# Kernel tuning notes

Measured on AMD Instinct MI355X. Metric: run time of the kernel, lower is better.

The kernel has to match this reference:

```python
import jax, jax.numpy as jnp
import numpy as np


def setup_inputs() -> dict:
    key = jax.random.key(0)
    ks = jax.random.split(key, 6)
    B, S, D_IN, D_OUT, E, R = 4, 2048, 4096, 4096, 8, 16
    x = jax.random.normal(ks[0], (B, S, D_IN), dtype=jnp.float32)
    probs = jax.random.uniform(ks[1], (B, E), dtype=jnp.float32)
    router_probs = probs / jnp.sum(probs, axis=-1, keepdims=True)
    weight = jax.random.normal(ks[2], (D_OUT, D_IN), dtype=jnp.float32) * 0.02
    bias = jax.random.normal(ks[3], (D_OUT,), dtype=jnp.float32) * 0.02
    lora_A = jax.random.normal(ks[4], (E, R, D_IN), dtype=jnp.float32) * 0.02
    lora_B = jax.random.normal(ks[5], (E, D_OUT, R), dtype=jnp.float32) * 0.02
    return {"x": x, "router_probs": router_probs, "weight": weight,
            "bias": bias, "lora_A": lora_A, "lora_B": lora_B}


def reference(x, router_probs, weight, bias, lora_A, lora_B):
    scaling = 2.0
    # base linear: [b,s,i] @ [o,i]^T + bias
    base_out = jnp.einsum('bsi,oi->bso', x, weight) + bias
    # low-rank per-expert projection: [b,s,e,r] (small: r=16)
    mid = jnp.einsum('bsi,eri->bser', x, lora_A)
    # weight by router probs (per batch, per expert) before up-projection
    mid_w = mid * router_probs[:, None, :, None]
    # sum over experts fused into the up-projection contraction
    delta = jnp.einsum('bser,eor->bso', mid_w, lora_B) * scaling
    return base_out + delta
```

## Files before the change

kernel.cpp:

```cpp
#include <hip/hip_runtime.h>


typedef _Float16 half8 __attribute__((ext_vector_type(8)));
typedef _Float16 half4 __attribute__((ext_vector_type(4)));
typedef float    f32x4 __attribute__((ext_vector_type(4)));

#define M_TOT 8192
#define N_TOT 4096
#define K_IN  4096
#define KA    4224
#define NT    132

__device__ __forceinline__ void cvt_store4(_Float16* p, float4 f) {
  half4 h;
  h[0] = (_Float16)f.x; h[1] = (_Float16)f.y;
  h[2] = (_Float16)f.z; h[3] = (_Float16)f.w;
  *(half4*)p = h;
}

template <int LOG2C, int DCOLS>
__global__ __launch_bounds__(256) void convert_f32_f16_t(
    const float* __restrict__ src, _Float16* __restrict__ dst, int total8) {
  for (int i = blockIdx.x * 256 + threadIdx.x; i < total8;
       i += gridDim.x * 256) {
    int base = i << 3;
    int r = base >> LOG2C;
    int c = base & ((1 << LOG2C) - 1);
    const float4* s = (const float4*)(src + (size_t)base);
    float4 f0 = s[0], f1 = s[1];
    half8 h;
    h[0]=(_Float16)f0.x; h[1]=(_Float16)f0.y; h[2]=(_Float16)f0.z; h[3]=(_Float16)f0.w;
    h[4]=(_Float16)f1.x; h[5]=(_Float16)f1.y; h[6]=(_Float16)f1.z; h[7]=(_Float16)f1.w;
    *(half8*)(dst + (size_t)r * DCOLS + c) = h;
  }
}

__global__ __launch_bounds__(256) void wtail_gather_f16(
    const float* __restrict__ loraB, _Float16* __restrict__ Wa) {
  int idx = blockIdx.x * 256 + threadIdx.x;
  int n = idx >> 7, j = idx & 127;
  int e = j >> 4, r = j & 15;
  Wa[(size_t)n * KA + K_IN + j] =
      (_Float16)loraB[((size_t)e * N_TOT + n) * 16 + r];
}

__global__ __launch_bounds__(256) void lorabf_gather_f32(
    const float* __restrict__ loraB, float* __restrict__ lorabf) {
  int idx = blockIdx.x * 256 + threadIdx.x;
  int n = idx >> 7, j = idx & 127;
  int e = j >> 4, r = j & 15;
  lorabf[(size_t)n * 128 + j] = loraB[((size_t)e * N_TOT + n) * 16 + r];
}

__global__ __launch_bounds__(256) void mid2_kernel(
    _Float16* __restrict__ Xa, const _Float16* __restrict__ lAh,
    const float* __restrict__ router) {
  __shared__ _Float16 As[32 * 64];
  __shared__ _Float16 Bs[128 * 64];
  int tid = threadIdx.x, lane = tid & 63, w = tid >> 6;
  int m0 = blockIdx.x * 32;
  int b = m0 >> 11;
  f32x4 acc[2][2] = {};

  for (int ks = 0; ks < 64; ++ks) {
    int kb = ks * 128;
    {
      const char* s = (const char*)Xa +
          (size_t)(m0 + w * 8 + (lane >> 3)) * (KA * 2) + kb + (lane & 7) * 16;
      __builtin_amdgcn_global_load_lds(
          (const __attribute__((address_space(1))) void*)s,
          (__attribute__((address_space(3))) void*)((char*)As + w * 1024), 16, 0, 0);
    }
#pragma unroll
    for (int i = 0; i < 4; ++i) {
      const char* s = (const char*)lAh +
          (size_t)((w * 4 + i) * 8 + (lane >> 3)) * (4096 * 2) + kb + (lane & 7) * 16;
      __builtin_amdgcn_global_load_lds(
          (const __attribute__((address_space(1))) void*)s,
          (__attribute__((address_space(3))) void*)((char*)Bs + (w * 4 + i) * 1024), 16, 0, 0);
    }
    __syncthreads();
#pragma unroll
    for (int kk = 0; kk < 2; ++kk) {
      half8 a[2], bf[2];
#pragma unroll
      for (int mi = 0; mi < 2; ++mi)
        a[mi] = *(const half8*)(As + (mi * 16 + (lane & 15)) * 64 + kk * 32 + (lane >> 4) * 8);
#pragma unroll
      for (int ni = 0; ni < 2; ++ni)
        bf[ni] = *(const half8*)(Bs + (w * 32 + ni * 16 + (lane & 15)) * 64 + kk * 32 + (lane >> 4) * 8);
#pragma unroll
      for (int mi = 0; mi < 2; ++mi)
#pragma unroll
        for (int ni = 0; ni < 2; ++ni)
          acc[mi][ni] = __builtin_amdgcn_mfma_f32_16x16x32_f16(a[mi], bf[ni], acc[mi][ni], 0, 0, 0);
    }
    __syncthreads();
  }

#pragma unroll
  for (int ni = 0; ni < 2; ++ni) {
    int j = w * 32 + ni * 16 + (lane & 15);
    int e = j >> 4;
    float sc = 2.0f * router[b * 8 + e];
#pragma unroll
    for (int mi = 0; mi < 2; ++mi) {
      f32x4 v = acc[mi][ni];
#pragma unroll
      for (int jj = 0; jj < 4; ++jj) {
        int m = m0 + mi * 16 + (lane >> 4) * 4 + jj;
        Xa[(size_t)m * KA + K_IN + j] = (_Float16)(v[jj] * sc);
      }
    }
  }
}

__global__ __launch_bounds__(256) void mid_kernel(
    const float* __restrict__ x, const float* __restrict__ loraA,
    const float* __restrict__ router, float* __restrict__ midw) {
  __shared__ _Float16 As[32 * 64];
  __shared__ _Float16 Bs[128 * 64];
  int tid = threadIdx.x, lane = tid & 63, w = tid >> 6;
  int m0 = blockIdx.x * 32;
  int b = m0 >> 11;
  f32x4 acc[2][2] = {};
  for (int ks = 0; ks < 64; ++ks) {
    int k0 = ks * 64;
#pragma unroll
    for (int it = 0; it < 2; ++it) {
      int idx = tid + it * 256;
      int r = idx >> 4, c4 = idx & 15;
      float4 f = *(const float4*)(x + (size_t)(m0 + r) * K_IN + k0 + c4 * 4);
      cvt_store4(As + r * 64 + c4 * 4, f);
    }
#pragma unroll
    for (int it = 0; it < 8; ++it) {
      int idx = tid + it * 256;
      int r = idx >> 4, c4 = idx & 15;
      float4 f = *(const float4*)(loraA + (size_t)r * K_IN + k0 + c4 * 4);
      cvt_store4(Bs + r * 64 + c4 * 4, f);
    }
    __syncthreads();
#pragma unroll
    for (int kk = 0; kk < 2; ++kk) {
      half8 a[2], bf[2];
#pragma unroll
      for (int mi = 0; mi < 2; ++mi)
        a[mi] = *(const half8*)(As + (mi * 16 + (lane & 15)) * 64 + kk * 32 + (lane >> 4) * 8);
#pragma unroll
      for (int ni = 0; ni < 2; ++ni)
        bf[ni] = *(const half8*)(Bs + (w * 32 + ni * 16 + (lane & 15)) * 64 + kk * 32 + (lane >> 4) * 8);
#pragma unroll
      for (int mi = 0; mi < 2; ++mi)
#pragma unroll
        for (int ni = 0; ni < 2; ++ni)
          acc[mi][ni] = __builtin_amdgcn_mfma_f32_16x16x32_f16(a[mi], bf[ni], acc[mi][ni], 0, 0, 0);
    }
    __syncthreads();
  }
#pragma unroll
  for (int ni = 0; ni < 2; ++ni) {
    int j = w * 32 + ni * 16 + (lane & 15);
    int e = j >> 4;
    float sc = 2.0f * router[b * 8 + e];
#pragma unroll
    for (int mi = 0; mi < 2; ++mi) {
      f32x4 v = acc[mi][ni];
#pragma unroll
      for (int jj = 0; jj < 4; ++jj) {
        int m = m0 + mi * 16 + (lane >> 4) * 4 + jj;
        midw[(size_t)m * 128 + j] = v[jj] * sc;
      }
    }
  }
}

#define BAR    __builtin_amdgcn_s_barrier()
#define SCHED0 __builtin_amdgcn_sched_barrier(0)
#define PRIO1  __builtin_amdgcn_s_setprio(1)
#define PRIO0  __builtin_amdgcn_s_setprio(0)
#define VMW0   asm volatile("s_waitcnt vmcnt(0)" ::: "memory")
#define GLOAD(src, dst) __builtin_amdgcn_global_load_lds( \
    (const __attribute__((address_space(1))) void*)(src), \
    (__attribute__((address_space(3))) void*)(dst), 16, 0, 0)

#define READS(AF, BF, SL) do { \
  _Pragma("unroll") for (int ni = 0; ni < 4; ++ni) \
    BF[ni] = *(const half8*)(LDS + 65536 + (SL) * 16384 + \
                             (wn + ni * 16 + ln15) * 64 + rslot); \
  _Pragma("unroll") for (int mi = 0; mi < 8; ++mi) \
    AF[mi] = *(const half8*)(LDS + (SL) * 16384 + \
                             (wm + mi * 16 + ln15) * 64 + rslot); \
  } while (0)

#define STAGE4(TT, SL) do { \
  const char* sA_ = XpC + (size_t)(TT) * 64; \
  const char* sB_ = WpC + (size_t)(TT) * 64; \
  GLOAD(sA_ + goff0, LDS + (SL) * 16384 + l0); \
  GLOAD(sA_ + goff1, LDS + (SL) * 16384 + l1); \
  GLOAD(sB_ + goff0, LDS + 65536 + (SL) * 16384 + l0); \
  GLOAD(sB_ + goff1, LDS + 65536 + (SL) * 16384 + l1); \
  } while (0)

#define MFMA32(AF, BF) do { \
  PRIO1; \
  _Pragma("unroll") for (int mi = 0; mi < 8; ++mi) \
    _Pragma("unroll") for (int ni = 0; ni < 4; ++ni) \
      acc[mi][ni] = __builtin_amdgcn_mfma_f32_16x16x32_f16( \
          AF[mi], BF[ni], acc[mi][ni], 0, 0, 0); \
  PRIO0; \
  } while (0)

#define TILE_NB(AF, BF, SL) do { READS(AF, BF, SL); MFMA32(AF, BF); } while (0)

__global__ __launch_bounds__(512, 2) void gemm256(
    const _Float16* __restrict__ Xa, const _Float16* __restrict__ Wa,
    const float* __restrict__ bias, float* __restrict__ out) {
  __shared__ __align__(16) char LDS[131072];

  int tid = threadIdx.x, lane = tid & 63, w = tid >> 6;
  int ln15 = lane & 15, ln4 = lane >> 4;
  int wm = (w >> 2) * 128, wn = (w & 3) * 64;

  int bid = blockIdx.x;
  int xcd = bid & 7, idx = bid >> 3;
  int mt = (xcd & 3) * 8 + (idx & 7);
  int nt = (xcd >> 2) * 8 + (idx >> 3);
  int m0 = mt << 8, n0 = nt << 8;

  const char* XpC = (const char*)Xa + (size_t)m0 * (KA * 2);
  const char* WpC = (const char*)Wa + (size_t)n0 * (KA * 2);

  int i0 = tid, i1 = tid + 512;
  int goff0 = (i0 >> 2) * (KA * 2) + (((i0 & 3) ^ ((i0 >> 3) & 3)) * 16);
  int goff1 = (i1 >> 2) * (KA * 2) + (((i1 & 3) ^ ((i1 >> 3) & 3)) * 16);
  int l0 = i0 * 16, l1 = i1 * 16;

  int rslot = ((ln4 ^ ((lane >> 1) & 3)) * 16);

  f32x4 acc[8][4] = {};
  half8 aE[8], bE[4], aO[8], bO[4];

  STAGE4(0, 0); STAGE4(1, 1);

#pragma unroll 1
  for (int t4 = 0; t4 < NT; t4 += 4) {
    VMW0; BAR; SCHED0;
    STAGE4(t4 + 2, 2); STAGE4(t4 + 3, 3);
    TILE_NB(aE, bE, 0);
    TILE_NB(aO, bO, 1);
    VMW0; BAR; SCHED0;
    if (t4 + 4 < NT) { STAGE4(t4 + 4, 0); STAGE4(t4 + 5, 1); }
    TILE_NB(aE, bE, 2);
    TILE_NB(aO, bO, 3);
  }

#pragma unroll
  for (int ni = 0; ni < 4; ++ni) {
    int n = n0 + wn + ni * 16 + ln15;
    float bz = bias[n];
#pragma unroll
    for (int mi = 0; mi < 8; ++mi) {
      f32x4 v = acc[mi][ni];
      int mb = m0 + wm + mi * 16 + ln4 * 4;
#pragma unroll
      for (int jj = 0; jj < 4; ++jj)
        out[(size_t)(mb + jj) * N_TOT + n] = v[jj] + bz;
    }
  }
}

__global__ __launch_bounds__(256) void gemm_fallback(
    const float* __restrict__ x, const float* __restrict__ wgt,
    const float* __restrict__ midw, const float* __restrict__ lorabf,
    const float* __restrict__ bias, float* __restrict__ out) {
  __shared__ _Float16 As[128 * 64];
  __shared__ _Float16 Bs[128 * 64];
  int tid = threadIdx.x, lane = tid & 63, w = tid >> 6;
  int mt = blockIdx.x & 63, nt = blockIdx.x >> 6;
  int m0 = mt << 7, n0 = nt << 7;
  int wm = (w >> 1) * 64, wn = (w & 1) * 64;
  f32x4 acc[4][4] = {};
  for (int ks = 0; ks < 66; ++ks) {
    int k0 = ks * 64;
    const float *asrc, *bsrc; size_t astr, bstr; int ac, bc;
    if (ks < 64) { asrc = x;    astr = K_IN; ac = k0;        bsrc = wgt;    bstr = K_IN; bc = k0; }
    else         { asrc = midw; astr = 128;  ac = k0 - K_IN; bsrc = lorabf; bstr = 128;  bc = k0 - K_IN; }
#pragma unroll
    for (int it = 0; it < 8; ++it) {
      int idx = tid + it * 256;
      int r = idx >> 4, c4 = idx & 15;
      float4 fa = *(const float4*)(asrc + (size_t)(m0 + r) * astr + ac + c4 * 4);
      cvt_store4(As + r * 64 + c4 * 4, fa);
      float4 fb = *(const float4*)(bsrc + (size_t)(n0 + r) * bstr + bc + c4 * 4);
      cvt_store4(Bs + r * 64 + c4 * 4, fb);
    }
    __syncthreads();
#pragma unroll
    for (int kk = 0; kk < 2; ++kk) {
      half8 a[4], bf[4];
#pragma unroll
      for (int mi = 0; mi < 4; ++mi)
        a[mi] = *(const half8*)(As + (wm + mi * 16 + (lane & 15)) * 64 + kk * 32 + (lane >> 4) * 8);
#pragma unroll
      for (int ni = 0; ni < 4; ++ni)
        bf[ni] = *(const half8*)(Bs + (wn + ni * 16 + (lane & 15)) * 64 + kk * 32 + (lane >> 4) * 8);
#pragma unroll
      for (int mi = 0; mi < 4; ++mi)
#pragma unroll
        for (int ni = 0; ni < 4; ++ni)
          acc[mi][ni] = __builtin_amdgcn_mfma_f32_16x16x32_f16(a[mi], bf[ni], acc[mi][ni], 0, 0, 0);
    }
    __syncthreads();
  }
#pragma unroll
  for (int ni = 0; ni < 4; ++ni) {
    int n = n0 + wn + ni * 16 + (lane & 15);
    float bz = bias[n];
#pragma unroll
    for (int mi = 0; mi < 4; ++mi) {
      f32x4 v = acc[mi][ni];
      int mbase = m0 + wm + mi * 16 + (lane >> 4) * 4;
#pragma unroll
      for (int jj = 0; jj < 4; ++jj)
        out[(size_t)(mbase + jj) * N_TOT + n] = v[jj] + bz;
    }
  }
}

extern "C" void kernel_launch(void* const* d_in, const int* in_sizes, int n_in,
                              void* d_out, int out_size, void* d_ws, size_t ws_size,
                              hipStream_t stream) {
  const float* x      = (const float*)d_in[0];
  const float* router = (const float*)d_in[1];
  const float* wgt    = (const float*)d_in[2];
  const float* bias   = (const float*)d_in[3];
  const float* loraA  = (const float*)d_in[4];
  const float* loraB  = (const float*)d_in[5];
  float* out = (float*)d_out;
  char* ws = (char*)d_ws;

  const size_t XAUG_B = (size_t)M_TOT * KA * 2;
  const size_t WAUG_B = (size_t)N_TOT * KA * 2;
  const size_t LAH_B  = (size_t)128 * K_IN * 2;
  const size_t MIDW_B = (size_t)M_TOT * 128 * 4;
  bool fast = ws_size >= XAUG_B + WAUG_B + LAH_B;

  if (fast) {
    _Float16* Xa  = (_Float16*)ws;
    _Float16* Wa  = (_Float16*)(ws + XAUG_B);
    _Float16* lAh = (_Float16*)(ws + XAUG_B + WAUG_B);
    convert_f32_f16_t<12, KA><<<2048, 256, 0, stream>>>(x,   Xa, M_TOT * K_IN / 8);
    convert_f32_f16_t<12, KA><<<2048, 256, 0, stream>>>(wgt, Wa, N_TOT * K_IN / 8);
    convert_f32_f16_t<12, 4096><<<256, 256, 0, stream>>>(loraA, lAh, 128 * K_IN / 8);
    wtail_gather_f16<<<2048, 256, 0, stream>>>(loraB, Wa);
    mid2_kernel<<<256, 256, 0, stream>>>(Xa, lAh, router);
    gemm256<<<512, 512, 0, stream>>>(Xa, Wa, bias, out);
  } else {
    float* midw   = (float*)ws;
    float* lorabf = (float*)(ws + MIDW_B);
    lorabf_gather_f32<<<2048, 256, 0, stream>>>(loraB, lorabf);
    mid_kernel<<<256, 256, 0, stream>>>(x, loraA, router, midw);
    gemm_fallback<<<2048, 256, 0, stream>>>(x, wgt, midw, lorabf, bias, out);
  }
}
```

Measured before the change: 379.2 us.

## Stream GEMM B operand from global to registers and deepen A LDS pipeline

In the main GEMM kernel, the weight (B) tiles now load straight from global memory into registers one tile ahead. Only the activation (A) tiles are staged through LDS, in a four-slot ring with one barrier per k-tile, and LDS shrinks to 64KB. A fragments are read in two halves to save registers. Separately, the mid2 kernel gets an XOR-swizzled LDS layout to cut bank conflicts on its fragment reads. The trade-off is that waves sharing a column block now fetch B redundantly from cache. The loop also relies on implicit compiler waitcnts, not explicit vmcnt waits, to order the LDS-bound loads.

After: 486.8 us. 28.4% more time.

```diff
diff --git a/kernel.cpp b/kernel.cpp
--- a/kernel.cpp
+++ b/kernel.cpp
@@ -62,33 +62,37 @@
   int b = m0 >> 11;
   f32x4 acc[2][2] = {};
 
+  int scol = ((lane & 7) ^ (lane >> 3)) * 16;
+  int ln15 = lane & 15, ln4 = lane >> 4;
+
   for (int ks = 0; ks < 64; ++ks) {
     int kb = ks * 128;
     {
       const char* s = (const char*)Xa +
-          (size_t)(m0 + w * 8 + (lane >> 3)) * (KA * 2) + kb + (lane & 7) * 16;
+          (size_t)(m0 + w * 8 + (lane >> 3)) * (KA * 2) + kb + scol;
       __builtin_amdgcn_global_load_lds(
           (const __attribute__((address_space(1))) void*)s,
-          (__attribute__((address_space(3))) void*)((char*)As + w * 1024), 16, 0, 0);
+          (__attribute__((address_space(3))) void*)((char*)As + w * 1024 + lane * 16), 16, 0, 0);
     }
 #pragma unroll
     for (int i = 0; i < 4; ++i) {
       const char* s = (const char*)lAh +
-          (size_t)((w * 4 + i) * 8 + (lane >> 3)) * (4096 * 2) + kb + (lane & 7) * 16;
+          (size_t)((w * 4 + i) * 8 + (lane >> 3)) * (4096 * 2) + kb + scol;
       __builtin_amdgcn_global_load_lds(
           (const __attribute__((address_space(1))) void*)s,
-          (__attribute__((address_space(3))) void*)((char*)Bs + (w * 4 + i) * 1024), 16, 0, 0);
+          (__attribute__((address_space(3))) void*)((char*)Bs + (w * 4 + i) * 1024 + lane * 16), 16, 0, 0);
     }
     __syncthreads();
 #pragma unroll
     for (int kk = 0; kk < 2; ++kk) {
+      int rs = (((kk * 4 + ln4) ^ (ln15 & 7)) << 4);
       half8 a[2], bf[2];
 #pragma unroll
       for (int mi = 0; mi < 2; ++mi)
-        a[mi] = *(const half8*)(As + (mi * 16 + (lane & 15)) * 64 + kk * 32 + (lane >> 4) * 8);
+        a[mi] = *(const half8*)((const char*)As + (mi * 16 + ln15) * 128 + rs);
 #pragma unroll
       for (int ni = 0; ni < 2; ++ni)
-        bf[ni] = *(const half8*)(Bs + (w * 32 + ni * 16 + (lane & 15)) * 64 + kk * 32 + (lane >> 4) * 8);
+        bf[ni] = *(const half8*)((const char*)Bs + (w * 32 + ni * 16 + ln15) * 128 + rs);
 #pragma unroll
       for (int mi = 0; mi < 2; ++mi)
 #pragma unroll
@@ -100,7 +104,7 @@
 
 #pragma unroll
   for (int ni = 0; ni < 2; ++ni) {
-    int j = w * 32 + ni * 16 + (lane & 15);
+    int j = w * 32 + ni * 16 + ln15;
     int e = j >> 4;
     float sc = 2.0f * router[b * 8 + e];
 #pragma unroll
@@ -108,7 +112,7 @@
       f32x4 v = acc[mi][ni];
 #pragma unroll
       for (int jj = 0; jj < 4; ++jj) {
-        int m = m0 + mi * 16 + (lane >> 4) * 4 + jj;
+        int m = m0 + mi * 16 + ln4 * 4 + jj;
         Xa[(size_t)m * KA + K_IN + j] = (_Float16)(v[jj] * sc);
       }
     }
@@ -179,44 +183,52 @@
 #define SCHED0 __builtin_amdgcn_sched_barrier(0)
 #define PRIO1  __builtin_amdgcn_s_setprio(1)
 #define PRIO0  __builtin_amdgcn_s_setprio(0)
-#define VMW0   asm volatile("s_waitcnt vmcnt(0)" ::: "memory")
+#define VMW4   asm volatile("s_waitcnt vmcnt(4)" ::: "memory")
 #define GLOAD(src, dst) __builtin_amdgcn_global_load_lds( \
     (const __attribute__((address_space(1))) void*)(src), \
     (__attribute__((address_space(3))) void*)(dst), 16, 0, 0)
 
-#define READS(AF, BF, SL) do { \
+#define READ_A4(mb, SL) do { \
+  _Pragma("unroll") for (int i = 0; i < 4; ++i) \
+    aF[i] = *(const half8*)(LDS + (SL) * 16384 + \
+                            (wm + ((mb) + i) * 16 + ln15) * 64 + rslot); \
+  } while (0)
+
+#define LOADB(BF, TT) do { \
+  const char* sB_ = WpC + (size_t)(TT) * 64; \
   _Pragma("unroll") for (int ni = 0; ni < 4; ++ni) \
-    BF[ni] = *(const half8*)(LDS + 65536 + (SL) * 16384 + \
-                             (wn + ni * 16 + ln15) * 64 + rslot); \
-  _Pragma("unroll") for (int mi = 0; mi < 8; ++mi) \
-    AF[mi] = *(const half8*)(LDS + (SL) * 16384 + \
-                             (wm + mi * 16 + ln15) * 64 + rslot); \
-  } while (0)
-
-#define STAGE4(TT, SL) do { \
+    BF[ni] = *(const half8*)(sB_ + boff[ni]); \
+  } while (0)
+
+#define MFMA16(mb, BF) do { \
+  PRIO1; \
+  _Pragma("unroll") for (int i = 0; i < 4; ++i) \
+    _Pragma("unroll") for (int ni = 0; ni < 4; ++ni) \
+      acc[(mb) + i][ni] = __builtin_amdgcn_mfma_f32_16x16x32_f16( \
+          aF[i], BF[ni], acc[(mb) + i][ni], 0, 0, 0); \
+  PRIO0; \
+  } while (0)
+
+#define STAGE_A(TT, SL) do { \
   const char* sA_ = XpC + (size_t)(TT) * 64; \
-  const char* sB_ = WpC + (size_t)(TT) * 64; \
   GLOAD(sA_ + goff0, LDS + (SL) * 16384 + l0); \
   GLOAD(sA_ + goff1, LDS + (SL) * 16384 + l1); \
-  GLOAD(sB_ + goff0, LDS + 65536 + (SL) * 16384 + l0); \
-  GLOAD(sB_ + goff1, LDS + 65536 + (SL) * 16384 + l1); \
-  } while (0)
-
-#define MFMA32(AF, BF) do { \
-  PRIO1; \
-  _Pragma("unroll") for (int mi = 0; mi < 8; ++mi) \
-    _Pragma("unroll") for (int ni = 0; ni < 4; ++ni) \
-      acc[mi][ni] = __builtin_amdgcn_mfma_f32_16x16x32_f16( \
-          AF[mi], BF[ni], acc[mi][ni], 0, 0, 0); \
-  PRIO0; \
-  } while (0)
-
-#define TILE_NB(AF, BF, SL) do { READS(AF, BF, SL); MFMA32(AF, BF); } while (0)
+  } while (0)
+
+#define TILE_T(SL, BCUR, BNXT) do { \
+  STAGE_A(t4 + (SL) + 3, ((SL) + 3) & 3); \
+  LOADB(BNXT, t4 + (SL) + 1); \
+  READ_A4(0, SL); \
+  MFMA16(0, BCUR); \
+  READ_A4(4, SL); \
+  MFMA16(4, BCUR); \
+  BAR; SCHED0; \
+  } while (0)
 
 __global__ __launch_bounds__(512, 2) void gemm256(
     const _Float16* __restrict__ Xa, const _Float16* __restrict__ Wa,
     const float* __restrict__ bias, float* __restrict__ out) {
-  __shared__ __align__(16) char LDS[131072];
+  __shared__ __align__(16) char LDS[65536];
 
   int tid = threadIdx.x, lane = tid & 63, w = tid >> 6;
   int ln15 = lane & 15, ln4 = lane >> 4;
@@ -238,22 +250,33 @@
 
   int rslot = ((ln4 ^ ((lane >> 1) & 3)) * 16);
 
+  int boff[4];
+#pragma unroll
+  for (int ni = 0; ni < 4; ++ni)
+    boff[ni] = (wn + ni * 16 + ln15) * (KA * 2) + ln4 * 16;
+
   f32x4 acc[8][4] = {};
-  half8 aE[8], bE[4], aO[8], bO[4];
-
-  STAGE4(0, 0); STAGE4(1, 1);
+  half8 aF[4], bE[4], bO[4];
+
+  LOADB(bE, 0);
+  STAGE_A(0, 0); STAGE_A(1, 1); STAGE_A(2, 2);
+  VMW4; BAR; SCHED0;
 
 #pragma unroll 1
-  for (int t4 = 0; t4 < NT; t4 += 4) {
-    VMW0; BAR; SCHED0;
-    STAGE4(t4 + 2, 2); STAGE4(t4 + 3, 3);
-    TILE_NB(aE, bE, 0);
-    TILE_NB(aO, bO, 1);
-    VMW0; BAR; SCHED0;
-    if (t4 + 4 < NT) { STAGE4(t4 + 4, 0); STAGE4(t4 + 5, 1); }
-    TILE_NB(aE, bE, 2);
-    TILE_NB(aO, bO, 3);
-  }
+  for (int t4 = 0; t4 < NT - 4; t4 += 4) {
+    TILE_T(0, bE, bO);
+    TILE_T(1, bO, bE);
+    TILE_T(2, bE, bO);
+    TILE_T(3, bO, bE);
+  }
+
+  { STAGE_A(131, 3); LOADB(bO, 129);
+    READ_A4(0, 0); MFMA16(0, bE); READ_A4(4, 0); MFMA16(4, bE); BAR; SCHED0; }
+  { LOADB(bE, 130);
+    READ_A4(0, 1); MFMA16(0, bO); READ_A4(4, 1); MFMA16(4, bO); BAR; SCHED0; }
+  { LOADB(bO, 131);
+    READ_A4(0, 2); MFMA16(0, bE); READ_A4(4, 2); MFMA16(4, bE); BAR; SCHED0; }
+  { READ_A4(0, 3); MFMA16(0, bO); READ_A4(4, 3); MFMA16(4, bO); }
 
 #pragma unroll
   for (int ni = 0; ni < 4; ++ni) {
```
